# Performance work log

Hardware: AMD Instinct MI355X
Metric: run time of the kernel (lower is better)

The kernel has to match this reference:

```python
import jax, jax.numpy as jnp
import numpy as np

ROI = 268
K = 32
SLOPE = 0.33
EPS = 1e-5

def leaky(h):
    return jnp.where(h >= 0, h, SLOPE * h)

def bn(h, g, b):
    # BatchNorm in training mode: biased batch statistics over the node/batch axis
    mu = h.mean(0)
    var = ((h - mu) ** 2).mean(0)
    return (h - mu) * jax.lax.rsqrt(var + EPS) * g + b


def setup_inputs():
    B, F, C, deg = 64, ROI, 32, 32
    N = B * ROI
    key = jax.random.key(0)
    ks = jax.random.split(key, 32)
    x = jax.random.normal(ks[0], (N, F), jnp.float32)
    # static within-graph edges: every node has exactly `deg` incoming edges
    tgt = jnp.repeat(jnp.arange(N, dtype=jnp.int32), deg)
    src = (tgt // ROI) * ROI + jax.random.randint(ks[1], (N * deg,), 0, ROI, dtype=jnp.int32)
    edge_index = jnp.stack([src, tgt])
    batch = jnp.repeat(jnp.arange(B, dtype=jnp.int32), ROI)
    def lin(k, i, o):
        return 0.05 * jax.random.normal(k, (i, o), jnp.float32)
    def vec(k, o):
        return 0.05 * jax.random.normal(k, (o,), jnp.float32)
    p = dict(
        x=x, edge_index=edge_index, batch=batch,
        W1a=lin(ks[2], 2 * F, C), b1a=vec(ks[3], C), W1b=lin(ks[4], C, C), b1b=vec(ks[5], C),
        g1=1.0 + vec(ks[6], C), be1=vec(ks[7], C),
        W2a=lin(ks[8], 2 * F, C), b2a=vec(ks[9], C), W2b=lin(ks[10], C, C), b2b=vec(ks[11], C),
        g2=1.0 + vec(ks[12], C), be2=vec(ks[13], C),
        W3=lin(ks[14], 2 * F, 1), b3=vec(ks[15], 1), g3=1.0 + vec(ks[16], 1), be3=vec(ks[17], 1),
        Wl1=lin(ks[18], ROI + 2 * C, 256), bl1=vec(ks[19], 256), g4=1.0 + vec(ks[20], 256), be4=vec(ks[21], 256),
        Wl2=lin(ks[22], 256, 128), bl2=vec(ks[23], 128), g5=1.0 + vec(ks[24], 128), be5=vec(ks[25], 128),
        Wl3=lin(ks[26], 128, 1), bl3=vec(ks[27], 1),
    )
    return p


def reference(x, edge_index, batch,
              W1a, b1a, W1b, b1b, g1, be1,
              W2a, b2a, W2b, b2b, g2, be2,
              W3, b3, g3, be3,
              Wl1, bl1, g4, be4, Wl2, bl2, g5, be5, Wl3, bl3):
    N, F = x.shape
    B = N // ROI
    src, tgt = edge_index[0], edge_index[1]
    xi = x[tgt]                       # [E, F] central node feature
    xd = x[src] - xi                  # [E, F] x_j - x_i
    # --- gcn1: EdgeConv(mlp1) + BN + LeakyReLU (dropout = identity in eval) ---
    m1 = leaky(xi @ W1a[:F] + xd @ W1a[F:] + b1a) @ W1b + b1b   # [E, C]
    a1 = jax.ops.segment_max(m1, tgt, num_segments=N)
    a1 = jnp.where(jnp.isfinite(a1), a1, 0.0)
    x1 = leaky(bn(a1, g1, be1))
    # --- gcn3: EdgeConv(mlp3) + BN + LeakyReLU ---
    m3 = xi @ W3[:F] + xd @ W3[F:] + b3                          # [E, 1]
    a3 = jax.ops.segment_max(m3, tgt, num_segments=N)
    a3 = jnp.where(jnp.isfinite(a3), a3, 0.0)
    x3 = leaky(bn(a3, g3, be3))
    # --- gcn2: DynamicEdgeConv(mlp2, k=32) + BN + LeakyReLU ---
    xg = x.reshape(B, ROI, F)
    sq = jnp.sum(xg * xg, -1)
    d2 = sq[:, :, None] + sq[:, None, :] - 2.0 * jnp.einsum('bif,bjf->bij', xg, xg)
    _, idx = jax.lax.top_k(-d2, K)                               # [B, ROI, K], includes self
    xj = jax.vmap(lambda f, i: f[i])(xg, idx)                    # [B, ROI, K, F]
    part_i = jnp.einsum('bif,fc->bic', xg, W2a[:F])
    part_d = jnp.einsum('bikf,fc->bikc', xj - xg[:, :, None, :], W2a[F:])
    h2 = leaky(part_i[:, :, None, :] + part_d + b2a)
    m2 = h2 @ W2b + b2b                                          # [B, ROI, K, C]
    x2 = leaky(bn(m2.max(axis=2).reshape(N, -1), g2, be2))
    # --- readout ---
    counts = jax.ops.segment_sum(jnp.ones((N, 1), x.dtype), batch, num_segments=B)
    p1 = jax.ops.segment_sum(x1, batch, num_segments=B) / counts
    p2 = jax.ops.segment_sum(x2, batch, num_segments=B) / counts
    z = jnp.concatenate([p1, p2, x3.reshape(B, ROI)], -1)        # [B, 268+64]
    z = leaky(bn(z @ Wl1 + bl1, g4, be4))
    z = leaky(bn(z @ Wl2 + bl2, g5, be5))
    return z @ Wl3 + bl3                                          # [B, 1]
```

## Files before the change

### kernel.cpp

```cpp
#include <hip/hip_runtime.h>
#include <hip/hip_bf16.h>

#define ROI   268
#define FDIM  268
#define NB    64
#define NN    (NB*ROI)
#define CC    32
#define DEG   32
#define KSEL  32
#define SLOPE 0.33f
#define EPSBN 1e-5f

typedef __attribute__((ext_vector_type(8)))  short bf16x8;
typedef __attribute__((ext_vector_type(4)))  float f32x4;
typedef __attribute__((ext_vector_type(16))) float f32x16;

__device__ __forceinline__ float lrelu(float h) { return h >= 0.f ? h : SLOPE * h; }

__device__ __forceinline__ unsigned short f2bf(float f) {
    union { __hip_bfloat16 h; unsigned short s; } u;
    u.h = __float2bfloat16(f);
    return u.s;
}
__device__ __forceinline__ float bf2f(unsigned short h) {
    return __uint_as_float(((unsigned int)h) << 16);
}

#define PREP_PACK_BLOCKS  2448
#define PREP_PACKW_BLOCKS 18
#define PREP_SCAL_BLOCKS  1072

__global__ __launch_bounds__(256) void k_prep(
    const float* __restrict__ x,
    const float* __restrict__ W1a, const float* __restrict__ W2a,
    const float* __restrict__ W3,  const float* __restrict__ b3,
    unsigned short* __restrict__ Xh, unsigned short* __restrict__ Xl,
    unsigned short* __restrict__ Wfh, unsigned short* __restrict__ Wfl,
    float* __restrict__ u3, float* __restrict__ v3, float* __restrict__ sqv)
{
    const int bid = blockIdx.x;
    const int tid = threadIdx.x;
    if (bid < PREP_PACK_BLOCKS) {
        const int gid = bid * 256 + tid;
        const int l   = gid & 63;
        const int f3  = gid >> 6;
        const int ks  = f3 % 9;
        const int bc  = f3 / 9;
        const int ct  = bc % 17;
        const int b   = bc / 17;
        const int node = ct * 16 + (l & 15);
        const int k0   = ks * 32 + (l >> 4) * 8;
        float f[8];
        #pragma unroll
        for (int j = 0; j < 8; ++j) f[j] = 0.f;
        if (node < ROI) {
            const float* row = &x[((size_t)b * ROI + node) * FDIM];
            if (k0 + 3 < FDIM) { float4 v = *(const float4*)&row[k0];     f[0]=v.x; f[1]=v.y; f[2]=v.z; f[3]=v.w; }
            if (k0 + 7 < FDIM) { float4 v = *(const float4*)&row[k0 + 4]; f[4]=v.x; f[5]=v.y; f[6]=v.z; f[7]=v.w; }
        }
        unsigned short hh[8], ll[8];
        #pragma unroll
        for (int j = 0; j < 8; ++j) {
            hh[j] = f2bf(f[j]);
            ll[j] = f2bf(f[j] - bf2f(hh[j]));
        }
        uint4 hp, lp;
        hp.x = (unsigned)hh[0] | ((unsigned)hh[1] << 16); hp.y = (unsigned)hh[2] | ((unsigned)hh[3] << 16);
        hp.z = (unsigned)hh[4] | ((unsigned)hh[5] << 16); hp.w = (unsigned)hh[6] | ((unsigned)hh[7] << 16);
        lp.x = (unsigned)ll[0] | ((unsigned)ll[1] << 16); lp.y = (unsigned)ll[2] | ((unsigned)ll[3] << 16);
        lp.z = (unsigned)ll[4] | ((unsigned)ll[5] << 16); lp.w = (unsigned)ll[6] | ((unsigned)ll[7] << 16);
        const size_t base = (size_t)f3 * 512 + l * 8;
        *(uint4*)&Xh[base] = hp;
        *(uint4*)&Xl[base] = lp;
    } else if (bid < PREP_PACK_BLOCKS + PREP_PACKW_BLOCKS) {
        const int gid = (bid - PREP_PACK_BLOCKS) * 256 + tid;
        const int l  = gid & 63;
        const int f3 = gid >> 6;
        const int ks = f3 % 9;
        const int mc = f3 / 9;
        const int ct = mc & 1;
        const int m  = mc >> 1;
        const int k0 = ks * 32 + (l >> 4) * 8;
        const int c  = ct * 16 + (l & 15);
        const float* W = (m < 2) ? W1a : W2a;
        const bool isU = (m & 1) == 0;
        unsigned short hh[8], ll[8];
        #pragma unroll
        for (int j = 0; j < 8; ++j) {
            const int kk = k0 + j;
            float val = 0.f;
            if (kk < FDIM) {
                float wb = W[(size_t)(FDIM + kk) * CC + c];
                val = isU ? (W[(size_t)kk * CC + c] - wb) : wb;
            }
            hh[j] = f2bf(val);
            ll[j] = f2bf(val - bf2f(hh[j]));
        }
        uint4 hp, lp;
        hp.x = (unsigned)hh[0] | ((unsigned)hh[1] << 16); hp.y = (unsigned)hh[2] | ((unsigned)hh[3] << 16);
        hp.z = (unsigned)hh[4] | ((unsigned)hh[5] << 16); hp.w = (unsigned)hh[6] | ((unsigned)hh[7] << 16);
        lp.x = (unsigned)ll[0] | ((unsigned)ll[1] << 16); lp.y = (unsigned)ll[2] | ((unsigned)ll[3] << 16);
        lp.z = (unsigned)ll[4] | ((unsigned)ll[5] << 16); lp.w = (unsigned)ll[6] | ((unsigned)ll[7] << 16);
        const size_t base = (size_t)f3 * 512 + l * 8;
        *(uint4*)&Wfh[base] = hp;
        *(uint4*)&Wfl[base] = lp;
    } else {
        const int s = bid - (PREP_PACK_BLOCKS + PREP_PACKW_BLOCKS);
        const int l = tid & 63;
        #pragma unroll
        for (int i = 0; i < 4; ++i) {
            const int n = s * 16 + i * 4 + (tid >> 6);
            const float* row = &x[(size_t)n * FDIM];
            float su = 0.f, sv = 0.f, sq = 0.f;
            #pragma unroll
            for (int t = 0; t < 4; ++t) {
                const int f = l + 64 * t;
                float xv = row[f];
                float wv = W3[FDIM + f];
                float wu = W3[f] - wv;
                su += xv * wu; sv += xv * wv; sq += xv * xv;
            }
            if (l < 12) {
                const int f = 256 + l;
                float xv = row[f];
                float wv = W3[FDIM + f];
                float wu = W3[f] - wv;
                su += xv * wu; sv += xv * wv; sq += xv * xv;
            }
            #pragma unroll
            for (int mm = 32; mm > 0; mm >>= 1) {
                su += __shfl_xor(su, mm);
                sv += __shfl_xor(sv, mm);
                sq += __shfl_xor(sq, mm);
            }
            if (l == 0) {
                u3[n] = su + b3[0];
                v3[n] = sv;
                sqv[n] = sq;
            }
        }
    }
}

#define PD_DIST_BLOCKS 192
#define PD_PROJ_BLOCKS 1088

__global__ __launch_bounds__(512) void k_projdist(
    const unsigned short* __restrict__ Xh, const unsigned short* __restrict__ Xl,
    const unsigned short* __restrict__ Wfh, const unsigned short* __restrict__ Wfl,
    const float* __restrict__ b1a, const float* __restrict__ b2a,
    const float* __restrict__ sqv,
    float* __restrict__ u1, float* __restrict__ v1,
    float* __restrict__ u2, float* __restrict__ v2,
    float* __restrict__ d2)
{
    __shared__ __align__(16) unsigned short Bh_l[4608], Bl_l[4608];
    __shared__ float sqj[288];
    const int tid = threadIdx.x;
    const int l   = tid & 63;
    const int w   = tid >> 6;

    if (blockIdx.x >= PD_DIST_BLOCKS) {
        const int tile = blockIdx.x - PD_DIST_BLOCKS;
        const int b    = tile / 17;
        const int ctn  = tile % 17;
        const int m    = w >> 1;
        const int ct   = w & 1;
        bf16x8 Ah[9], Al[9];
        {
            const size_t abase = (size_t)tile * 9 * 512 + l * 8;
            #pragma unroll
            for (int ks = 0; ks < 9; ++ks) {
                Ah[ks] = *(const bf16x8*)&Xh[abase + ks * 512];
                Al[ks] = *(const bf16x8*)&Xl[abase + ks * 512];
            }
        }
        float* outp = (m == 0) ? u1 : (m == 1) ? v1 : (m == 2) ? u2 : v2;
        const size_t wbase = ((size_t)((m * 2 + ct) * 9)) * 512 + l * 8;
        f32x4 acc = {0.f, 0.f, 0.f, 0.f};
        #pragma unroll
        for (int ks = 0; ks < 9; ++ks) {
            bf16x8 bh = *(const bf16x8*)&Wfh[wbase + ks * 512];
            bf16x8 bl = *(const bf16x8*)&Wfl[wbase + ks * 512];
            acc = __builtin_amdgcn_mfma_f32_16x16x32_bf16(Ah[ks], bh, acc, 0, 0, 0);
            acc = __builtin_amdgcn_mfma_f32_16x16x32_bf16(Ah[ks], bl, acc, 0, 0, 0);
            acc = __builtin_amdgcn_mfma_f32_16x16x32_bf16(Al[ks], bh, acc, 0, 0, 0);
        }
        const int ch = ct * 16 + (l & 15);
        float bias = 0.f;
        if (m == 0) bias = b1a[ch];
        else if (m == 2) bias = b2a[ch];
        const int r0 = (l >> 4) * 4;
        #pragma unroll
        for (int i = 0; i < 4; ++i) {
            const int node = ctn * 16 + r0 + i;
            if (node < ROI)
                outp[((size_t)b * ROI + node) * 32 + ch] = acc[i] + bias;
        }
        return;
    }

    const int bid = blockIdx.x;
    const int b   = bid / 3;
    const int bx  = bid % 3;
    const int at  = min(bx * 8 + w, 16);
    const size_t bN = (size_t)b * ROI;

    for (int t = tid; t < 288; t += 512)
        sqj[t] = (t < ROI) ? sqv[bN + t] : __builtin_inff();

    bf16x8 Ah[9], Al[9];
    {
        const size_t abase = ((size_t)(b * 17 + at) * 9) * 512 + l * 8;
        #pragma unroll
        for (int ks = 0; ks < 9; ++ks) {
            Ah[ks] = *(const bf16x8*)&Xh[abase + ks * 512];
            Al[ks] = *(const bf16x8*)&Xl[abase + ks * 512];
        }
    }
    const int rbase = at * 16 + (l >> 4) * 4;
    float sqr4[4];
    #pragma unroll
    for (int i = 0; i < 4; ++i) {
        const int row = rbase + i;
        sqr4[i] = (row < ROI) ? sqv[bN + row] : 0.f;
    }

    float* drow = &d2[(size_t)b * 288 * 288];
    for (int ct = 0; ct < 17; ++ct) {
        __syncthreads();
        {
            const unsigned short* srcH = &Xh[((size_t)(b * 17 + ct) * 9) * 512];
            const unsigned short* srcL = &Xl[((size_t)(b * 17 + ct) * 9) * 512];
            for (int t = tid; t < 576; t += 512) {
                *(uint4*)&Bh_l[t * 8] = *(const uint4*)&srcH[t * 8];
                *(uint4*)&Bl_l[t * 8] = *(const uint4*)&srcL[t * 8];
            }
        }
        __syncthreads();
        f32x4 acc = {0.f, 0.f, 0.f, 0.f};
        #pragma unroll
        for (int ks = 0; ks < 9; ++ks) {
            bf16x8 bh = *(const bf16x8*)&Bh_l[ks * 512 + l * 8];
            bf16x8 bl = *(const bf16x8*)&Bl_l[ks * 512 + l * 8];
            acc = __builtin_amdgcn_mfma_f32_16x16x32_bf16(Ah[ks], bh, acc, 0, 0, 0);
            acc = __builtin_amdgcn_mfma_f32_16x16x32_bf16(Ah[ks], bl, acc, 0, 0, 0);
            acc = __builtin_amdgcn_mfma_f32_16x16x32_bf16(Al[ks], bh, acc, 0, 0, 0);
        }
        const int col = ct * 16 + (l & 15);
        const float sj = sqj[col];
        #pragma unroll
        for (int i = 0; i < 4; ++i)
            drow[(size_t)(rbase + i) * 288 + col] = sqr4[i] + sj - 2.f * acc[i];
    }
    for (int t = tid; t < 128 * 16; t += 512) {
        const int r = bx * 128 + (t >> 4);
        if (r < 288) drow[(size_t)r * 288 + 272 + (t & 15)] = __builtin_inff();
    }
}

#define EDGE_GROUPS 10
#define EDGE_NPB 27
#define VSH 40

__global__ __launch_bounds__(256) void k_edge_fused(
    const float* __restrict__ u1, const float* __restrict__ v1,
    const float* __restrict__ W1b, const float* __restrict__ b1b,
    const int* __restrict__ ei,
    const float* __restrict__ u2, const float* __restrict__ v2,
    const float* __restrict__ W2b, const float* __restrict__ b2b,
    const float* __restrict__ d2,
    const float* __restrict__ u3, const float* __restrict__ v3,
    float* __restrict__ a1, float* __restrict__ a2, float* __restrict__ a3)
{
    __shared__ __align__(16) unsigned short vs[ROI * VSH];
    __shared__ float vs3[ROI];
    __shared__ int jn_l[EDGE_NPB][32];

    const int tid  = threadIdx.x;
    const int l    = tid & 63;
    const int wv   = tid >> 6;
    const int half = l >> 5;
    const int e    = l & 31;
    const bool g1  = blockIdx.x < (NB * EDGE_GROUPS);
    const int rem  = g1 ? blockIdx.x : blockIdx.x - NB * EDGE_GROUPS;
    const int b    = rem / EDGE_GROUPS;
    const int q    = rem % EDGE_GROUPS;
    const int n0   = q * EDGE_NPB;
    const int cnt  = min(EDGE_NPB, ROI - n0);
    const size_t bN = (size_t)b * ROI;

    const float* u  = g1 ? u1 : u2;
    const float* v  = g1 ? v1 : v2;
    const float* Wb = g1 ? W1b : W2b;
    const float* bb = g1 ? b1b : b2b;
    float* aout     = g1 ? a1 : a2;

    {
        const float* vsrc = v + bN * 32;
        for (int i = tid * 4; i < ROI * 32; i += 1024) {
            float4 vv = *(const float4*)&vsrc[i];
            const int r = i >> 5, c0 = i & 31;
            uint2 p;
            p.x = (unsigned)f2bf(vv.x) | ((unsigned)f2bf(vv.y) << 16);
            p.y = (unsigned)f2bf(vv.z) | ((unsigned)f2bf(vv.w) << 16);
            *(uint2*)&vs[r * VSH + c0] = p;
        }
        if (g1)
            for (int t = tid; t < ROI; t += 256) vs3[t] = v3[bN + t];
    }

    union { bf16x8 v8; unsigned u4[4]; } B0, B1;
    #pragma unroll
    for (int j = 0; j < 4; ++j) {
        B0.u4[j] = (unsigned)f2bf(Wb[(half * 8 + 2*j    ) * 32 + e])
                 | ((unsigned)f2bf(Wb[(half * 8 + 2*j + 1) * 32 + e]) << 16);
        B1.u4[j] = (unsigned)f2bf(Wb[(16 + half * 8 + 2*j    ) * 32 + e])
                 | ((unsigned)f2bf(Wb[(16 + half * 8 + 2*j + 1) * 32 + e]) << 16);
    }
    const float biasc = bb[e];

    if (!g1) {
        const int grp8 = tid >> 5;
        const int sl   = tid & 31;
        for (int r2 = 0; r2 < 4; ++r2) {
            const int il = grp8 + 8 * r2;
            if (il >= cnt) break;
            const float* src = &d2[(size_t)b * 288 * 288 + (size_t)(n0 + il) * 288];
            unsigned k[9];
            #pragma unroll
            for (int qq = 0; qq < 9; ++qq) {
                const int idx = qq * 32 + sl;
                unsigned bits = __float_as_uint(src[idx]);
                unsigned msk  = (unsigned)(((int)bits) >> 31) | 0x80000000u;
                k[qq] = ((bits ^ msk) & ~0x1FFu) | (unsigned)idx;
            }
            #pragma unroll
            for (int i = 1; i < 9; ++i) {
                #pragma unroll
                for (int j = i; j > 0; --j) {
                    unsigned lo = k[j-1] < k[j] ? k[j-1] : k[j];
                    unsigned hi = k[j-1] < k[j] ? k[j]   : k[j-1];
                    k[j-1] = lo; k[j] = hi;
                }
            }
            unsigned keep = 0;
            #pragma unroll
            for (int it = 0; it < KSEL; ++it) {
                unsigned m = k[0];
                #pragma unroll
                for (int mm = 16; mm > 0; mm >>= 1) {
                    unsigned o = (unsigned)__shfl_xor((int)m, mm, 32);
                    m = o < m ? o : m;
                }
                if (sl == it) keep = m;
                const bool win = (k[0] == m);
                #pragma unroll
                for (int qq = 0; qq < 8; ++qq) k[qq] = win ? k[qq+1] : k[qq];
                k[8] = win ? 0xFFFFFFFFu : k[8];
            }
            jn_l[il][sl] = (int)(keep & 0x1FFu);
        }
    }
    __syncthreads();

    for (int il = wv; il < cnt; il += 4) {
        const int n  = (int)bN + n0 + il;
        const int jnl = g1 ? (ei[(size_t)n * DEG + e] - (int)bN) : jn_l[il][e];

        float hv[16];
        #pragma unroll
        for (int s = 0; s < 2; ++s) {
            const int c0 = s * 16 + half * 8;
            float4 uv0 = *(const float4*)&u[(size_t)n * 32 + c0];
            float4 uv1 = *(const float4*)&u[(size_t)n * 32 + c0 + 4];
            bf16x8 vb = *(const bf16x8*)&vs[jnl * VSH + c0];
            const unsigned short* vbs = (const unsigned short*)&vb;
            hv[s*8+0] = lrelu(uv0.x + bf2f(vbs[0]));
            hv[s*8+1] = lrelu(uv0.y + bf2f(vbs[1]));
            hv[s*8+2] = lrelu(uv0.z + bf2f(vbs[2]));
            hv[s*8+3] = lrelu(uv0.w + bf2f(vbs[3]));
            hv[s*8+4] = lrelu(uv1.x + bf2f(vbs[4]));
            hv[s*8+5] = lrelu(uv1.y + bf2f(vbs[5]));
            hv[s*8+6] = lrelu(uv1.z + bf2f(vbs[6]));
            hv[s*8+7] = lrelu(uv1.w + bf2f(vbs[7]));
        }
        union { bf16x8 v8; unsigned u4[4]; } A0, A1;
        #pragma unroll
        for (int j = 0; j < 4; ++j) {
            A0.u4[j] = (unsigned)f2bf(hv[2*j])     | ((unsigned)f2bf(hv[2*j + 1]) << 16);
            A1.u4[j] = (unsigned)f2bf(hv[8 + 2*j]) | ((unsigned)f2bf(hv[8 + 2*j + 1]) << 16);
        }
        f32x16 acc = {0.f,0.f,0.f,0.f,0.f,0.f,0.f,0.f,0.f,0.f,0.f,0.f,0.f,0.f,0.f,0.f};
        acc = __builtin_amdgcn_mfma_f32_32x32x16_bf16(A0.v8, B0.v8, acc, 0, 0, 0);
        acc = __builtin_amdgcn_mfma_f32_32x32x16_bf16(A1.v8, B1.v8, acc, 0, 0, 0);

        float mx = acc[0];
        #pragma unroll
        for (int r = 1; r < 16; ++r) mx = fmaxf(mx, acc[r]);
        mx = fmaxf(mx, __shfl_xor(mx, 32));
        if (l < 32) aout[(size_t)n * 32 + l] = mx + biasc;

        if (g1) {
            float a3v = u3[n] + vs3[jnl];
            #pragma unroll
            for (int mm = 16; mm > 0; mm >>= 1) a3v = fmaxf(a3v, __shfl_xor(a3v, mm));
            if (l == 0) a3[n] = a3v;
        }
    }
}

__global__ __launch_bounds__(256) void k_stats1(
    const float* __restrict__ a1, const float* __restrict__ a2,
    float* __restrict__ part)
{
    const int p = blockIdx.x;
    const int tid = threadIdx.x;
    const int ch = tid & 31, sub = tid >> 5;
    const size_t base = (size_t)p * ROI;
    float s1 = 0.f, q1 = 0.f, s2 = 0.f, q2 = 0.f;
    for (int n = sub; n < ROI; n += 8) {
        float v1 = a1[(base + n) * 32 + ch];
        float v2 = a2[(base + n) * 32 + ch];
        s1 += v1; q1 += v1 * v1; s2 += v2; q2 += v2 * v2;
    }
    __shared__ float L[4][256];
    L[0][tid] = s1; L[1][tid] = q1; L[2][tid] = s2; L[3][tid] = q2;
    __syncthreads();
    if (tid < 128) {
        const int a = tid >> 5, c = tid & 31;
        float s = 0.f;
        #pragma unroll
        for (int k = 0; k < 8; ++k) s += L[a][c + 32 * k];
        part[p * 128 + a * 32 + c] = s;
    }
}

__global__ __launch_bounds__(256) void k_pool_fc1(
    const float* __restrict__ a1, const float* __restrict__ a2, const float* __restrict__ a3,
    const float* __restrict__ part,
    const float* __restrict__ g1, const float* __restrict__ be1,
    const float* __restrict__ g2, const float* __restrict__ be2,
    const float* __restrict__ g3, const float* __restrict__ be3,
    const float* __restrict__ Wl1, const float* __restrict__ bl1,
    float* __restrict__ h1)
{
    const int b = blockIdx.x, tid = threadIdx.x;
    __shared__ float stl[130];
    __shared__ float zs[332];
    __shared__ float P[4][64];
    __shared__ float S3[256], Q3[256];

    {
        float p0 = 0.f, p1 = 0.f, p2 = 0.f, p3 = 0.f;
        float q0 = 0.f, q1 = 0.f, q2 = 0.f, q3 = 0.f;
        int n = tid;
        for (; n + 768 < NN; n += 1024) {
            float a = a3[n], bb = a3[n + 256], c = a3[n + 512], d = a3[n + 768];
            p0 += a; q0 += a * a;
            p1 += bb; q1 += bb * bb;
            p2 += c; q2 += c * c;
            p3 += d; q3 += d * d;
        }
        for (; n < NN; n += 256) { float a = a3[n]; p0 += a; q0 += a * a; }
        S3[tid] = (p0 + p1) + (p2 + p3);
        Q3[tid] = (q0 + q1) + (q2 + q3);
    }
    __syncthreads();
    for (int off = 128; off > 0; off >>= 1) {
        if (tid < off) { S3[tid] += S3[tid + off]; Q3[tid] += Q3[tid + off]; }
        __syncthreads();
    }
    if (tid < 64) {
        const int a = (tid >> 5) * 2, c = tid & 31;
        float s0 = 0.f, s1 = 0.f, q0b = 0.f, q1b = 0.f;
        for (int p = 0; p < 64; p += 2) {
            s0  += part[p * 128 + a * 32 + c];
            q0b += part[p * 128 + (a + 1) * 32 + c];
            s1  += part[(p + 1) * 128 + a * 32 + c];
            q1b += part[(p + 1) * 128 + (a + 1) * 32 + c];
        }
        float ss = s0 + s1, qq = q0b + q1b;
        float gv = (tid < 32) ? g1[c] : g2[c];
        float bv = (tid < 32) ? be1[c] : be2[c];
        float mu  = ss * (1.f / NN);
        float var = qq * (1.f / NN) - mu * mu;
        float sc  = gv * rsqrtf(var + EPSBN);
        stl[tid * 2] = sc; stl[tid * 2 + 1] = bv - mu * sc;
    }
    if (tid == 64) {
        float mu  = S3[0] * (1.f / NN);
        float var = Q3[0] * (1.f / NN) - mu * mu;
        float sc  = g3[0] * rsqrtf(var + EPSBN);
        stl[128] = sc; stl[129] = be3[0] - mu * sc;
    }
    __syncthreads();

    const int c = tid & 63, grp = tid >> 6;
    const float* src = (c < 32) ? a1 : a2;
    const int ch = c & 31;
    const float sc = stl[c * 2], sh = stl[c * 2 + 1];
    {
        const size_t rb = (size_t)b * ROI;
        float p0 = 0.f, p1 = 0.f, p2 = 0.f, p3 = 0.f;
        int i = grp;
        for (; i + 12 < ROI; i += 16) {
            p0 += lrelu(src[(rb + i)      * 32 + ch] * sc + sh);
            p1 += lrelu(src[(rb + i + 4)  * 32 + ch] * sc + sh);
            p2 += lrelu(src[(rb + i + 8)  * 32 + ch] * sc + sh);
            p3 += lrelu(src[(rb + i + 12) * 32 + ch] * sc + sh);
        }
        for (; i < ROI; i += 4)
            p0 += lrelu(src[(rb + i) * 32 + ch] * sc + sh);
        P[grp][c] = (p0 + p1) + (p2 + p3);
    }
    const float sc3 = stl[128], sh3 = stl[129];
    for (int i = tid; i < ROI; i += 256)
        zs[64 + i] = lrelu(a3[b * ROI + i] * sc3 + sh3);
    __syncthreads();
    if (tid < 64)
        zs[tid] = (P[0][tid] + P[1][tid] + P[2][tid] + P[3][tid]) * (1.f / ROI);
    __syncthreads();

    {
        float s0 = 0.f, s1 = 0.f, s2 = 0.f, s3 = 0.f;
        #pragma unroll 4
        for (int k = 0; k < 332; k += 4) {
            s0 += zs[k]     * Wl1[(size_t)k       * 256 + tid];
            s1 += zs[k + 1] * Wl1[(size_t)(k + 1) * 256 + tid];
            s2 += zs[k + 2] * Wl1[(size_t)(k + 2) * 256 + tid];
            s3 += zs[k + 3] * Wl1[(size_t)(k + 3) * 256 + tid];
        }
        h1[(size_t)b * 256 + tid] = bl1[tid] + ((s0 + s1) + (s2 + s3));
    }
}

__global__ __launch_bounds__(128) void k_fc2s(
    const float* __restrict__ h1,
    const float* __restrict__ g4, const float* __restrict__ be4,
    const float* __restrict__ Wl2, const float* __restrict__ bl2,
    float* __restrict__ h2)
{
    const int b = blockIdx.x, tid = threadIdx.x;
    __shared__ float hs[256];
    float s0 = 0.f, q0 = 0.f, s1 = 0.f, q1 = 0.f;
    float s2 = 0.f, q2 = 0.f, s3 = 0.f, q3 = 0.f;
    for (int r = 0; r < NB; r += 2) {
        float a = h1[(size_t)r * 256 + tid];
        float c = h1[(size_t)r * 256 + tid + 128];
        float d = h1[(size_t)(r + 1) * 256 + tid];
        float e = h1[(size_t)(r + 1) * 256 + tid + 128];
        s0 += a; q0 += a * a;
        s1 += c; q1 += c * c;
        s2 += d; q2 += d * d;
        s3 += e; q3 += e * e;
    }
    {
        float ssA = s0 + s2, qqA = q0 + q2;
        float muA = ssA * (1.f / NB);
        float vaA = qqA * (1.f / NB) - muA * muA;
        float scA = g4[tid] * rsqrtf(vaA + EPSBN);
        float shA = be4[tid] - muA * scA;
        hs[tid] = lrelu(h1[(size_t)b * 256 + tid] * scA + shA);
        float ssB = s1 + s3, qqB = q1 + q3;
        float muB = ssB * (1.f / NB);
        float vaB = qqB * (1.f / NB) - muB * muB;
        float scB = g4[tid + 128] * rsqrtf(vaB + EPSBN);
        float shB = be4[tid + 128] - muB * scB;
        hs[tid + 128] = lrelu(h1[(size_t)b * 256 + tid + 128] * scB + shB);
    }
    __syncthreads();
    float s0b = 0.f, s1b = 0.f, s2b = 0.f, s3b = 0.f;
    #pragma unroll 4
    for (int k = 0; k < 256; k += 4) {
        s0b += hs[k]     * Wl2[(size_t)k       * 128 + tid];
        s1b += hs[k + 1] * Wl2[(size_t)(k + 1) * 128 + tid];
        s2b += hs[k + 2] * Wl2[(size_t)(k + 2) * 128 + tid];
        s3b += hs[k + 3] * Wl2[(size_t)(k + 3) * 128 + tid];
    }
    h2[(size_t)b * 128 + tid] = bl2[tid] + ((s0b + s1b) + (s2b + s3b));
}

__global__ __launch_bounds__(128) void k_fc3s(
    const float* __restrict__ h2,
    const float* __restrict__ g5, const float* __restrict__ be5,
    const float* __restrict__ Wl3, const float* __restrict__ bl3,
    float* __restrict__ out)
{
    const int tid = threadIdx.x;
    __shared__ float T[64][133];
    float s0 = 0.f, q0 = 0.f, s1 = 0.f, q1 = 0.f;
    for (int r = 0; r < NB; r += 2) {
        float a = h2[(size_t)r * 128 + tid];
        float b = h2[(size_t)(r + 1) * 128 + tid];
        s0 += a; q0 += a * a;
        s1 += b; q1 += b * b;
    }
    float ss = s0 + s1, qq = q0 + q1;
    float mu  = ss * (1.f / NB);
    float var = qq * (1.f / NB) - mu * mu;
    float sc  = g5[tid] * rsqrtf(var + EPSBN);
    float sh  = be5[tid] - mu * sc;
    const float w3 = Wl3[tid];
    for (int r = 0; r < NB; ++r)
        T[r][tid] = lrelu(h2[(size_t)r * 128 + tid] * sc + sh) * w3;
    __syncthreads();
    if (tid < 64) {
        float a0 = 0.f, a1 = 0.f, a2 = 0.f, a3 = 0.f;
        #pragma unroll 4
        for (int c = 0; c < 128; c += 4) {
            a0 += T[tid][c];
            a1 += T[tid][c + 1];
            a2 += T[tid][c + 2];
            a3 += T[tid][c + 3];
        }
        out[tid] = bl3[0] + ((a0 + a1) + (a2 + a3));
    }
}

extern "C" void kernel_launch(void* const* d_in, const int* in_sizes, int n_in,
                              void* d_out, int out_size, void* d_ws, size_t ws_size,
                              hipStream_t stream)
{
    (void)in_sizes; (void)n_in; (void)out_size; (void)ws_size;
    const float* x   = (const float*)d_in[0];
    const int*   ei  = (const int*)d_in[1];
    const float* W1a = (const float*)d_in[3];
    const float* b1a = (const float*)d_in[4];
    const float* W1b = (const float*)d_in[5];
    const float* b1b = (const float*)d_in[6];
    const float* g1  = (const float*)d_in[7];
    const float* be1 = (const float*)d_in[8];
    const float* W2a = (const float*)d_in[9];
    const float* b2a = (const float*)d_in[10];
    const float* W2b = (const float*)d_in[11];
    const float* b2b = (const float*)d_in[12];
    const float* g2  = (const float*)d_in[13];
    const float* be2 = (const float*)d_in[14];
    const float* W3  = (const float*)d_in[15];
    const float* b3  = (const float*)d_in[16];
    const float* g3  = (const float*)d_in[17];
    const float* be3 = (const float*)d_in[18];
    const float* Wl1 = (const float*)d_in[19];
    const float* bl1 = (const float*)d_in[20];
    const float* g4  = (const float*)d_in[21];
    const float* be4 = (const float*)d_in[22];
    const float* Wl2 = (const float*)d_in[23];
    const float* bl2 = (const float*)d_in[24];
    const float* g5  = (const float*)d_in[25];
    const float* be5 = (const float*)d_in[26];
    const float* Wl3 = (const float*)d_in[27];
    const float* bl3 = (const float*)d_in[28];

    float* ws  = (float*)d_ws;
    float* u1  = ws;
    float* v1  = u1 + (size_t)NN * 32;
    float* u2  = v1 + (size_t)NN * 32;
    float* v2  = u2 + (size_t)NN * 32;
    float* u3  = v2 + (size_t)NN * 32;
    float* v3  = u3 + NN;
    float* sqv = v3 + NN;
    float* a1  = sqv + NN;
    float* a2  = a1 + (size_t)NN * 32;
    float* a3  = a2 + (size_t)NN * 32;
    float* h1  = a3 + NN;
    float* h2  = h1 + (size_t)NB * 256;
    float* part = h2 + (size_t)NB * 128;
    unsigned short* Xh = (unsigned short*)(((uintptr_t)(part + 64 * 128) + 255) & ~(uintptr_t)255);
    unsigned short* Xl = Xh + (size_t)64 * 17 * 9 * 512;
    float* d2 = (float*)(((uintptr_t)(Xl + (size_t)64 * 17 * 9 * 512) + 255) & ~(uintptr_t)255);
    unsigned short* Wfh = (unsigned short*)(d2 + (size_t)64 * 288 * 288);
    unsigned short* Wfl = Wfh + (size_t)8 * 9 * 512;

    k_prep<<<PREP_PACK_BLOCKS + PREP_PACKW_BLOCKS + PREP_SCAL_BLOCKS, 256, 0, stream>>>(
        x, W1a, W2a, W3, b3, Xh, Xl, Wfh, Wfl, u3, v3, sqv);
    k_projdist<<<PD_DIST_BLOCKS + PD_PROJ_BLOCKS, 512, 0, stream>>>(
        Xh, Xl, Wfh, Wfl, b1a, b2a, sqv, u1, v1, u2, v2, d2);
    k_edge_fused<<<2 * NB * EDGE_GROUPS, 256, 0, stream>>>(
        u1, v1, W1b, b1b, ei, u2, v2, W2b, b2b, d2, u3, v3, a1, a2, a3);
    k_stats1<<<64, 256, 0, stream>>>(a1, a2, part);
    k_pool_fc1<<<NB, 256, 0, stream>>>(a1, a2, a3, part, g1, be1, g2, be2, g3, be3,
                                       Wl1, bl1, h1);
    k_fc2s<<<NB, 128, 0, stream>>>(h1, g4, be4, Wl2, bl2, h2);
    k_fc3s<<<1, 128, 0, stream>>>(h2, g5, be5, Wl3, bl3, (float*)d_out);
}
```

Measured before the change: 150.5 us.

## Fuse top-k neighbor selection into distance kernel, drop d2 buffer

```diff
diff --git a/kernel.cpp b/kernel.cpp
--- a/kernel.cpp
+++ b/kernel.cpp
@@ -142,7 +142,7 @@
     }
 }
 
-#define PD_DIST_BLOCKS 192
+#define PD_DIST_BLOCKS 576
 #define PD_PROJ_BLOCKS 1088
 
 __global__ __launch_bounds__(512) void k_projdist(
@@ -152,9 +152,9 @@
     const float* __restrict__ sqv,
     float* __restrict__ u1, float* __restrict__ v1,
     float* __restrict__ u2, float* __restrict__ v2,
-    float* __restrict__ d2)
-{
-    __shared__ __align__(16) unsigned short Bh_l[4608], Bl_l[4608];
+    int* __restrict__ knn)
+{
+    __shared__ float S[32][297];
     __shared__ float sqj[288];
     const int tid = threadIdx.x;
     const int l   = tid & 63;
@@ -201,14 +201,19 @@
     }
 
     const int bid = blockIdx.x;
-    const int b   = bid / 3;
-    const int bx  = bid % 3;
-    const int at  = min(bx * 8 + w, 16);
+    const int b   = bid / 9;
+    const int rt  = bid % 9;
+    const int r0g = rt * 32;
+    const int nrows = min(32, ROI - r0g);
     const size_t bN = (size_t)b * ROI;
 
     for (int t = tid; t < 288; t += 512)
         sqj[t] = (t < ROI) ? sqv[bN + t] : __builtin_inff();
-
+    for (int t = tid; t < 32 * 16; t += 512)
+        S[t >> 4][272 + (t & 15)] = __builtin_inff();
+
+    const int a  = w & 1;
+    const int at = min(rt * 2 + a, 16);
     bf16x8 Ah[9], Al[9];
     {
         const size_t abase = ((size_t)(b * 17 + at) * 9) * 512 + l * 8;
@@ -218,31 +223,21 @@
             Al[ks] = *(const bf16x8*)&Xl[abase + ks * 512];
         }
     }
-    const int rbase = at * 16 + (l >> 4) * 4;
+    const int rloc = (at - rt * 2) * 16 + (l >> 4) * 4;
     float sqr4[4];
     #pragma unroll
     for (int i = 0; i < 4; ++i) {
-        const int row = rbase + i;
+        const int row = r0g + rloc + i;
         sqr4[i] = (row < ROI) ? sqv[bN + row] : 0.f;
     }
 
-    float* drow = &d2[(size_t)b * 288 * 288];
-    for (int ct = 0; ct < 17; ++ct) {
-        __syncthreads();
-        {
-            const unsigned short* srcH = &Xh[((size_t)(b * 17 + ct) * 9) * 512];
-            const unsigned short* srcL = &Xl[((size_t)(b * 17 + ct) * 9) * 512];
-            for (int t = tid; t < 576; t += 512) {
-                *(uint4*)&Bh_l[t * 8] = *(const uint4*)&srcH[t * 8];
-                *(uint4*)&Bl_l[t * 8] = *(const uint4*)&srcL[t * 8];
-            }
-        }
-        __syncthreads();
+    for (int ct = (w >> 1); ct < 17; ct += 4) {
+        const size_t bbase = ((size_t)(b * 17 + ct) * 9) * 512 + l * 8;
         f32x4 acc = {0.f, 0.f, 0.f, 0.f};
         #pragma unroll
         for (int ks = 0; ks < 9; ++ks) {
-            bf16x8 bh = *(const bf16x8*)&Bh_l[ks * 512 + l * 8];
-            bf16x8 bl = *(const bf16x8*)&Bl_l[ks * 512 + l * 8];
+            bf16x8 bh = *(const bf16x8*)&Xh[bbase + ks * 512];
+            bf16x8 bl = *(const bf16x8*)&Xl[bbase + ks * 512];
             acc = __builtin_amdgcn_mfma_f32_16x16x32_bf16(Ah[ks], bh, acc, 0, 0, 0);
             acc = __builtin_amdgcn_mfma_f32_16x16x32_bf16(Ah[ks], bl, acc, 0, 0, 0);
             acc = __builtin_amdgcn_mfma_f32_16x16x32_bf16(Al[ks], bh, acc, 0, 0, 0);
@@ -251,11 +246,47 @@
         const float sj = sqj[col];
         #pragma unroll
         for (int i = 0; i < 4; ++i)
-            drow[(size_t)(rbase + i) * 288 + col] = sqr4[i] + sj - 2.f * acc[i];
-    }
-    for (int t = tid; t < 128 * 16; t += 512) {
-        const int r = bx * 128 + (t >> 4);
-        if (r < 288) drow[(size_t)r * 288 + 272 + (t & 15)] = __builtin_inff();
+            S[rloc + i][col] = sqr4[i] + sj - 2.f * acc[i];
+    }
+    __syncthreads();
+
+    const int grp = tid >> 5, sl = tid & 31;
+    for (int rr = 0; rr < 2; ++rr) {
+        const int row = grp + rr * 16;
+        if (row >= nrows) continue;
+        unsigned k[9];
+        #pragma unroll
+        for (int q = 0; q < 9; ++q) {
+            const int idx = q * 32 + sl;
+            unsigned bits = __float_as_uint(S[row][idx]);
+            unsigned msk  = (unsigned)(((int)bits) >> 31) | 0x80000000u;
+            k[q] = ((bits ^ msk) & ~0x1FFu) | (unsigned)idx;
+        }
+        #pragma unroll
+        for (int i = 1; i < 9; ++i) {
+            #pragma unroll
+            for (int j = i; j > 0; --j) {
+                unsigned lo = k[j-1] < k[j] ? k[j-1] : k[j];
+                unsigned hi = k[j-1] < k[j] ? k[j]   : k[j-1];
+                k[j-1] = lo; k[j] = hi;
+            }
+        }
+        unsigned keep = 0;
+        #pragma unroll
+        for (int it = 0; it < KSEL; ++it) {
+            unsigned m = k[0];
+            #pragma unroll
+            for (int mm = 16; mm > 0; mm >>= 1) {
+                unsigned o = (unsigned)__shfl_xor((int)m, mm, 32);
+                m = o < m ? o : m;
+            }
+            if (sl == it) keep = m;
+            const bool win = (k[0] == m);
+            #pragma unroll
+            for (int q = 0; q < 8; ++q) k[q] = win ? k[q+1] : k[q];
+            k[8] = win ? 0xFFFFFFFFu : k[8];
+        }
+        knn[(bN + r0g + row) * 32 + sl] = (int)bN + (int)(keep & 0x1FFu);
     }
 }
 
@@ -269,13 +300,12 @@
     const int* __restrict__ ei,
     const float* __restrict__ u2, const float* __restrict__ v2,
     const float* __restrict__ W2b, const float* __restrict__ b2b,
-    const float* __restrict__ d2,
+    const int* __restrict__ knn,
     const float* __restrict__ u3, const float* __restrict__ v3,
     float* __restrict__ a1, float* __restrict__ a2, float* __restrict__ a3)
 {
     __shared__ __align__(16) unsigned short vs[ROI * VSH];
     __shared__ float vs3[ROI];
-    __shared__ int jn_l[EDGE_NPB][32];
 
     const int tid  = threadIdx.x;
     const int l    = tid & 63;
@@ -294,6 +324,7 @@
     const float* v  = g1 ? v1 : v2;
     const float* Wb = g1 ? W1b : W2b;
     const float* bb = g1 ? b1b : b2b;
+    const int* nbr  = g1 ? ei : knn;
     float* aout     = g1 ? a1 : a2;
 
     {
@@ -320,70 +351,40 @@
     }
     const float biasc = bb[e];
 
-    if (!g1) {
-        const int grp8 = tid >> 5;
-        const int sl   = tid & 31;
-        for (int r2 = 0; r2 < 4; ++r2) {
-            const int il = grp8 + 8 * r2;
-            if (il >= cnt) break;
-            const float* src = &d2[(size_t)b * 288 * 288 + (size_t)(n0 + il) * 288];
-            unsigned k[9];
-            #pragma unroll
-            for (int qq = 0; qq < 9; ++qq) {
-                const int idx = qq * 32 + sl;
-                unsigned bits = __float_as_uint(src[idx]);
-                unsigned msk  = (unsigned)(((int)bits) >> 31) | 0x80000000u;
-                k[qq] = ((bits ^ msk) & ~0x1FFu) | (unsigned)idx;
-            }
-            #pragma unroll
-            for (int i = 1; i < 9; ++i) {
-                #pragma unroll
-                for (int j = i; j > 0; --j) {
-                    unsigned lo = k[j-1] < k[j] ? k[j-1] : k[j];
-                    unsigned hi = k[j-1] < k[j] ? k[j]   : k[j-1];
-                    k[j-1] = lo; k[j] = hi;
-                }
-            }
-            unsigned keep = 0;
-            #pragma unroll
-            for (int it = 0; it < KSEL; ++it) {
-                unsigned m = k[0];
-                #pragma unroll
-                for (int mm = 16; mm > 0; mm >>= 1) {
-                    unsigned o = (unsigned)__shfl_xor((int)m, mm, 32);
-                    m = o < m ? o : m;
-                }
-                if (sl == it) keep = m;
-                const bool win = (k[0] == m);
-                #pragma unroll
-                for (int qq = 0; qq < 8; ++qq) k[qq] = win ? k[qq+1] : k[qq];
-                k[8] = win ? 0xFFFFFFFFu : k[8];
-            }
-            jn_l[il][sl] = (int)(keep & 0x1FFu);
-        }
-    }
-    __syncthreads();
-
-    for (int il = wv; il < cnt; il += 4) {
-        const int n  = (int)bN + n0 + il;
-        const int jnl = g1 ? (ei[(size_t)n * DEG + e] - (int)bN) : jn_l[il][e];
+    int jns[8];
+    {
+        const int nper = (cnt + 3) >> 2;
+        #pragma unroll
+        for (int s = 0; s < 8; ++s) jns[s] = 0;
+        for (int s = 0; s < nper; ++s) {
+            const int il = wv + s * 4;
+            if (il < cnt)
+                jns[s] = nbr[(size_t)((int)bN + n0 + il) * DEG + e] - (int)bN;
+        }
+    }
+    __syncthreads();
+
+    int s = 0;
+    for (int il = wv; il < cnt; il += 4, ++s) {
+        const int n   = (int)bN + n0 + il;
+        const int jnl = jns[s];
 
         float hv[16];
         #pragma unroll
-        for (int s = 0; s < 2; ++s) {
-            const int c0 = s * 16 + half * 8;
+        for (int ss = 0; ss < 2; ++ss) {
+            const int c0 = ss * 16 + half * 8;
             float4 uv0 = *(const float4*)&u[(size_t)n * 32 + c0];
             float4 uv1 = *(const float4*)&u[(size_t)n * 32 + c0 + 4];
             bf16x8 vb = *(const bf16x8*)&vs[jnl * VSH + c0];
             const unsigned short* vbs = (const unsigned short*)&vb;
-            hv[s*8+0] = lrelu(uv0.x + bf2f(vbs[0]));
-            hv[s*8+1] = lrelu(uv0.y + bf2f(vbs[1]));
-            hv[s*8+2] = lrelu(uv0.z + bf2f(vbs[2]));
-            hv[s*8+3] = lrelu(uv0.w + bf2f(vbs[3]));
-            hv[s*8+4] = lrelu(uv1.x + bf2f(vbs[4]));
-            hv[s*8+5] = lrelu(uv1.y + bf2f(vbs[5]));
-            hv[s*8+6] = lrelu(uv1.z + bf2f(vbs[6]));
-            hv[s*8+7] = lrelu(uv1.w + bf2f(vbs[7]));
+            hv[ss*8+0] = lrelu(uv0.x + bf2f(vbs[0]));
+            hv[ss*8+1] = lrelu(uv0.y + bf2f(vbs[1]));
+            hv[ss*8+2] = lrelu(uv0.z + bf2f(vbs[2]));
+            hv[ss*8+3] = lrelu(uv0.w + bf2f(vbs[3]));
+            hv[ss*8+4] = lrelu(uv1.x + bf2f(vbs[4]));
+            hv[ss*8+5] = lrelu(uv1.y + bf2f(vbs[5]));
+            hv[ss*8+6] = lrelu(uv1.z + bf2f(vbs[6]));
+            hv[ss*8+7] = lrelu(uv1.w + bf2f(vbs[7]));
         }
         union { bf16x8 v8; unsigned u4[4]; } A0, A1;
         #pragma unroll
@@ -666,18 +667,18 @@
     float* h1  = a3 + NN;
     float* h2  = h1 + (size_t)NB * 256;
     float* part = h2 + (size_t)NB * 128;
-    unsigned short* Xh = (unsigned short*)(((uintptr_t)(part + 64 * 128) + 255) & ~(uintptr_t)255);
+    int*   knn = (int*)(part + 64 * 128);
+    unsigned short* Xh = (unsigned short*)(((uintptr_t)(knn + (size_t)NN * 32) + 255) & ~(uintptr_t)255);
     unsigned short* Xl = Xh + (size_t)64 * 17 * 9 * 512;
-    float* d2 = (float*)(((uintptr_t)(Xl + (size_t)64 * 17 * 9 * 512) + 255) & ~(uintptr_t)255);
-    unsigned short* Wfh = (unsigned short*)(d2 + (size_t)64 * 288 * 288);
+    unsigned short* Wfh = Xl + (size_t)64 * 17 * 9 * 512;
     unsigned short* Wfl = Wfh + (size_t)8 * 9 * 512;
 
     k_prep<<<PREP_PACK_BLOCKS + PREP_PACKW_BLOCKS + PREP_SCAL_BLOCKS, 256, 0, stream>>>(
         x, W1a, W2a, W3, b3, Xh, Xl, Wfh, Wfl, u3, v3, sqv);
     k_projdist<<<PD_DIST_BLOCKS + PD_PROJ_BLOCKS, 512, 0, stream>>>(
-        Xh, Xl, Wfh, Wfl, b1a, b2a, sqv, u1, v1, u2, v2, d2);
+        Xh, Xl, Wfh, Wfl, b1a, b2a, sqv, u1, v1, u2, v2, knn);
     k_edge_fused<<<2 * NB * EDGE_GROUPS, 256, 0, stream>>>(
-        u1, v1, W1b, b1b, ei, u2, v2, W2b, b2b, d2, u3, v3, a1, a2, a3);
+        u1, v1, W1b, b1b, ei, u2, v2, W2b, b2b, knn, u3, v3, a1, a2, a3);
     k_stats1<<<64, 256, 0, stream>>>(a1, a2, part);
     k_pool_fc1<<<NB, 256, 0, stream>>>(a1, a2, a3, part, g1, be1, g2, be2, g3, be3,
                                        Wl1, bl1, h1);
```

Result: no change. 149.1 us (-0.9%).
